# Performance work log

Measured on AMD Instinct MI355X. Metric: run time of the kernel, lower is better.

The kernel has to match this reference:

```python
import jax, jax.numpy as jnp
import numpy as np

DIM = 512
HEADS = 8
HEAD_DIM = 64
MAX_FREQ = 256.0


def axial_freqs(H, W, head_dim, max_freq=MAX_FREQ):
    # rotary-embedding-torch: per-axis rotary dim = head_dim // 2, freqs_for='pixel'
    r = head_dim // 2
    base = jnp.linspace(1.0, max_freq / 2.0, r // 2) * jnp.pi  # (r/2,)
    ph = jnp.linspace(-1.0, 1.0, H)
    pw = jnp.linspace(-1.0, 1.0, W)
    fh = jnp.repeat(ph[:, None] * base[None, :], 2, axis=-1)  # (H, r) interleaved repeat
    fw = jnp.repeat(pw[:, None] * base[None, :], 2, axis=-1)  # (W, r)
    fh = jnp.broadcast_to(fh[:, None, :], (H, W, r))
    fw = jnp.broadcast_to(fw[None, :, :], (H, W, r))
    return jnp.concatenate([fh, fw], axis=-1)  # (H, W, head_dim)


def rotate_half(t):
    # interleaved pairs: (x1, x2) -> (-x2, x1)
    shp = t.shape
    t = t.reshape(*shp[:-1], -1, 2)
    return jnp.stack((-t[..., 1], t[..., 0]), axis=-1).reshape(shp)


def apply_rope(t, freqs):
    # freqs: (H, W, d) broadcast over (BT, h, H, W, d)
    return t * jnp.cos(freqs) + rotate_half(t) * jnp.sin(freqs)


def setup_inputs() -> dict:
    key = jax.random.key(0)
    k1, k2, k3 = jax.random.split(key, 3)
    B, T, H, W, D = 2, 8, 32, 32, DIM
    inner = HEADS * HEAD_DIM
    x = jax.random.normal(k1, (B, T, H, W, D), dtype=jnp.float32)
    w_qkv = jax.random.normal(k2, (3 * inner, D), dtype=jnp.float32) * (D ** -0.5)
    w_out = jax.random.normal(k3, (D, inner), dtype=jnp.float32) * (inner ** -0.5)
    b_out = jnp.zeros((D,), dtype=jnp.float32)
    return {"x": x, "w_qkv": w_qkv, "w_out": w_out, "b_out": b_out}


def reference(x, w_qkv, w_out, b_out):
    B, T, H, W, D = x.shape
    h, d = HEADS, HEAD_DIM
    qkv = jnp.einsum('bthwc,fc->bthwf', x, w_qkv)  # (B,T,H,W,3*inner)
    q, k, v = jnp.split(qkv, 3, axis=-1)

    def to_heads(t):
        # B T H W (h d) -> (B T) h H W d
        t = t.reshape(B * T, H, W, h, d)
        return jnp.transpose(t, (0, 3, 1, 2, 4))

    q, k, v = to_heads(q), to_heads(k), to_heads(v)
    freqs = axial_freqs(H, W, d)
    q = apply_rope(q, freqs)
    k = apply_rope(k, freqs)

    q = q.reshape(B * T, h, H * W, d)
    k = k.reshape(B * T, h, H * W, d)
    v = v.reshape(B * T, h, H * W, d)

    scale = d ** -0.5
    logits = jnp.einsum('bhnd,bhmd->bhnm', q, k) * scale
    attn = jax.nn.softmax(logits, axis=-1)
    out = jnp.einsum('bhnm,bhmd->bhnd', attn, v)  # (BT, h, HW, d)

    # (B T) h (H W) d -> B T H W (h d)
    out = out.reshape(B, T, h, H, W, d)
    out = jnp.transpose(out, (0, 1, 3, 4, 2, 5)).reshape(B, T, H, W, h * d)
    return jnp.einsum('bthwf,df->bthwd', out, w_out) + b_out
```

## Files before the change

kernel.cpp:

```cpp
#include <hip/hip_runtime.h>
#include <math.h>

#define NH 8
#define HD 64
#define NSEQ 1024
#define DMODEL 512
#define F3 1536
#define NTOK 16384
#define BH 128
#define KVP 72
#define TP 136
#define QSCALE 0.1803368867f

typedef __attribute__((ext_vector_type(8))) short bf16x8;
typedef __attribute__((ext_vector_type(4))) float f32x4;
typedef __attribute__((ext_vector_type(16))) float f32x16;
typedef __attribute__((ext_vector_type(4))) unsigned int u32x4;
#define MFMA16(a, b, c) __builtin_amdgcn_mfma_f32_16x16x32_bf16(a, b, c, 0, 0, 0)
#define MFMA32(a, b, c) __builtin_amdgcn_mfma_f32_32x32x16_bf16(a, b, c, 0, 0, 0)

__device__ __forceinline__ float freq_of(int j) {
    return 3.14159265358979323846f * (1.0f + (float)j * (127.0f / 15.0f));
}
__device__ __forceinline__ unsigned short bf16_hi(float x) {
    unsigned u = __builtin_bit_cast(unsigned, x);
    return (unsigned short)(u >> 16);
}
__device__ __forceinline__ unsigned short bf16_rtn(float x) {
    unsigned u = __builtin_bit_cast(unsigned, x);
    return (unsigned short)((u + 0x7FFF + ((u >> 16) & 1)) >> 16);
}
__device__ __forceinline__ float bf16_tofloat(unsigned short h) {
    unsigned u = ((unsigned)h) << 16;
    return __builtin_bit_cast(float, u);
}
__device__ __forceinline__ int swz(int r) { return (r & 3) ^ ((r >> 2) & 3); }

__global__ __launch_bounds__(256) void split_kernel(
        const float* __restrict__ src, unsigned short* __restrict__ hi,
        unsigned short* __restrict__ lo) {
    const int i = blockIdx.x * 256 + threadIdx.x;
    const float4 v = ((const float4*)src)[i];
    ushort4 h, l;
    h.x = bf16_hi(v.x); l.x = bf16_hi(v.x - bf16_tofloat(h.x));
    h.y = bf16_hi(v.y); l.y = bf16_hi(v.y - bf16_tofloat(h.y));
    h.z = bf16_hi(v.z); l.z = bf16_hi(v.z - bf16_tofloat(h.z));
    h.w = bf16_hi(v.w); l.w = bf16_hi(v.w - bf16_tofloat(h.w));
    ((ushort4*)hi)[i] = h;
    ((ushort4*)lo)[i] = l;
}
__global__ __launch_bounds__(256) void cvt_kernel(
        const float* __restrict__ src, unsigned short* __restrict__ dst) {
    const int i = blockIdx.x * 256 + threadIdx.x;
    const float4 v = ((const float4*)src)[i];
    ((ushort4*)dst)[i] = make_ushort4(bf16_rtn(v.x), bf16_rtn(v.y),
                                      bf16_rtn(v.z), bf16_rtn(v.w));
}

template<int PLANES>
__device__ __forceinline__ void gemm_reg_pipe(
        const unsigned short* __restrict__ a_hi, const unsigned short* __restrict__ a_lo,
        const unsigned short* __restrict__ b_bf,
        char* lds, int m0, int f0, int t, f32x4 acc[4][4]) {
    const int w = t >> 6, lane = t & 63, l15 = lane & 15, quad = lane >> 4;
    const int mw = (w & 1) * 64, nw = (w >> 1) * 64;
    const int STAGE = PLANES * 4096;
    const int r = t >> 1;
    const int g0 = (t & 1) * 2;

    uint4 regs[PLANES][2];
    auto load_regs = [&](int kt) {
        const int k0 = kt * 32;
        #pragma unroll
        for (int p = 0; p < PLANES; p++) {
            const unsigned short* src =
                (p == 0) ? a_hi : ((p == PLANES - 1) ? b_bf : a_lo);
            const int row0 = (p == PLANES - 1) ? f0 : m0;
            const unsigned short* g = src + (size_t)(row0 + r) * DMODEL + k0 + g0 * 8;
            regs[p][0] = *(const uint4*)g;
            regs[p][1] = *(const uint4*)(g + 8);
        }
    };
    auto store_lds = [&](int stage) {
        unsigned short* S = (unsigned short*)lds + stage * STAGE;
        const int s0 = ((g0 ^ swz(r))) * 8;
        const int s1 = (((g0 + 1) ^ swz(r))) * 8;
        #pragma unroll
        for (int p = 0; p < PLANES; p++) {
            unsigned short* Sp = S + p * 4096 + r * 32;
            *(uint4*)&Sp[s0] = regs[p][0];
            *(uint4*)&Sp[s1] = regs[p][1];
        }
    };

    load_regs(0);
    store_lds(0);
    for (int kt = 0; kt < 16; kt++) {
        __syncthreads();
        if (kt < 15) load_regs(kt + 1);
        const unsigned short* S = (const unsigned short*)lds + (kt & 1) * STAGE;
        bf16x8 ah[4], al[4], bb[4];
        #pragma unroll
        for (int mt = 0; mt < 4; mt++) {
            const int rr = mw + mt * 16 + l15;
            const int off = rr * 32 + (quad ^ swz(rr)) * 8;
            ah[mt] = *(const bf16x8*)&S[off];
            if (PLANES == 3) al[mt] = *(const bf16x8*)&S[4096 + off];
        }
        #pragma unroll
        for (int nt = 0; nt < 4; nt++) {
            const int rr = nw + nt * 16 + l15;
            bb[nt] = *(const bf16x8*)&S[(PLANES - 1) * 4096 + rr * 32
                                        + (quad ^ swz(rr)) * 8];
        }
        #pragma unroll
        for (int mt = 0; mt < 4; mt++)
            #pragma unroll
            for (int nt = 0; nt < 4; nt++) {
                acc[mt][nt] = MFMA16(ah[mt], bb[nt], acc[mt][nt]);
                if (PLANES == 3) acc[mt][nt] = MFMA16(al[mt], bb[nt], acc[mt][nt]);
            }
        if (kt < 15) store_lds((kt + 1) & 1);
    }
    __syncthreads();
}

__global__ __launch_bounds__(256, 3) void qkv_mfma_kernel(
        const unsigned short* __restrict__ x_hi, const unsigned short* __restrict__ x_lo,
        const unsigned short* __restrict__ wq_bf,
        unsigned short* __restrict__ q_bf, unsigned short* __restrict__ k_bf,
        unsigned short* __restrict__ v_th) {
    __shared__ __align__(16) char lds[49152 + 4608];
    unsigned short* T = (unsigned short*)lds;
    float* t_cy = (float*)(lds + 49152);
    float* t_sy = t_cy + 64;
    float* t_cx = t_sy + 64;
    float* t_sx = t_cx + 512;

    const int m0 = blockIdx.x * 128;
    const int f0 = blockIdx.y * 128;
    const int t = threadIdx.x;
    const int w = t >> 6, lane = t & 63, l15 = lane & 15, quad = lane >> 4;
    const int mw = (w & 1) * 64, nw = (w >> 1) * 64;
    const int sel = f0 >> 9;
    const int bt = m0 >> 10;
    const int n0 = m0 & 1023;

    if (sel != 2) {
        for (int idx = t; idx < 576; idx += 256) {
            if (idx < 64) {
                const int yi = idx >> 4, j = idx & 15;
                const float pos = -1.0f + (float)((n0 >> 5) + yi) * (2.0f / 31.0f);
                float sv, cv; sincosf(pos * freq_of(j), &sv, &cv);
                t_sy[idx] = sv; t_cy[idx] = cv;
            } else {
                const int k2 = idx - 64, xi = k2 >> 4, j = k2 & 15;
                const float pos = -1.0f + (float)xi * (2.0f / 31.0f);
                float sv, cv; sincosf(pos * freq_of(j), &sv, &cv);
                t_sx[k2] = sv; t_cx[k2] = cv;
            }
        }
    }
    __syncthreads();

    f32x4 acc[4][4];
    #pragma unroll
    for (int mt = 0; mt < 4; mt++)
        #pragma unroll
        for (int nt = 0; nt < 4; nt++) acc[mt][nt] = (f32x4){0.f, 0.f, 0.f, 0.f};

    gemm_reg_pipe<3>(x_hi, x_lo, wq_bf, lds, m0, f0, t, acc);

    if (sel != 2) {
        const float post = (sel == 0) ? QSCALE : 1.0f;
        #pragma unroll
        for (int mt = 0; mt < 4; mt++)
            #pragma unroll
            for (int nt = 0; nt < 4; nt++)
                #pragma unroll
                for (int rr = 0; rr < 4; rr++) {
                    const int ml = mw + mt * 16 + quad * 4 + rr;
                    const int dd = (nw + nt * 16 + l15) & 63;
                    const int j0 = (dd & 31) >> 1;
                    float c, s;
                    if (dd < 32) { c = t_cy[(ml >> 5) * 16 + j0]; s = t_sy[(ml >> 5) * 16 + j0]; }
                    else         { c = t_cx[(ml & 31) * 16 + j0]; s = t_sx[(ml & 31) * 16 + j0]; }
                    const float v = acc[mt][nt][rr];
                    const float pv = __shfl_xor(v, 1);
                    acc[mt][nt][rr] = ((l15 & 1) ? (v * c + pv * s) : (v * c - pv * s)) * post;
                }
    }

    if (sel == 2) {
        #pragma unroll
        for (int mt = 0; mt < 4; mt++)
            #pragma unroll
            for (int nt = 0; nt < 4; nt++) {
                const int fl = nw + nt * 16 + l15;
                const int mlb = mw + mt * 16 + quad * 4;
                ushort4 pk = make_ushort4(
                    bf16_rtn(acc[mt][nt][0]), bf16_rtn(acc[mt][nt][1]),
                    bf16_rtn(acc[mt][nt][2]), bf16_rtn(acc[mt][nt][3]));
                *(ushort4*)&T[fl * TP + mlb] = pk;
            }
    } else {
        #pragma unroll
        for (int mt = 0; mt < 4; mt++)
            #pragma unroll
            for (int nt = 0; nt < 4; nt++)
                #pragma unroll
                for (int rr = 0; rr < 4; rr++) {
                    const int ml = mw + mt * 16 + quad * 4 + rr;
                    const int fl = nw + nt * 16 + l15;
                    T[ml * TP + fl] = bf16_rtn(acc[mt][nt][rr]);
                }
    }
    __syncthreads();
    if (sel == 2) {
        #pragma unroll
        for (int p = 0; p < 8; p++) {
            const int idx = p * 256 + t;
            const int fl = idx >> 4, g8 = (idx & 15) * 8;
            const int head = ((f0 + fl) >> 6) & 7;
            *(uint4*)(v_th + ((size_t)(bt * NH + head) * HD + ((f0 + fl) & 63)) * NSEQ
                      + n0 + g8) = *(const uint4*)&T[fl * TP + g8];
        }
    } else {
        unsigned short* dst = (sel == 0) ? q_bf : k_bf;
        #pragma unroll
        for (int p = 0; p < 8; p++) {
            const int idx = p * 256 + t;
            const int ml = idx >> 4, g8 = (idx & 15) * 8;
            const int head = ((f0 + g8) >> 6) & 7;
            *(uint4*)(dst + ((size_t)(bt * NH + head) * NSEQ + n0 + ml) * HD
                      + ((f0 + g8) & 63)) = *(const uint4*)&T[ml * TP + g8];
        }
    }
    __syncthreads();
}

__global__ __launch_bounds__(256, 3) void attn_kernel(
        const unsigned short* __restrict__ q_bf, const unsigned short* __restrict__ k_bf,
        const unsigned short* __restrict__ v_th,
        unsigned short* __restrict__ o_bf) {
    __shared__ unsigned short Ks[2][64 * KVP];
    __shared__ unsigned short Vs[2][64 * KVP];

    const int bh = blockIdx.x;
    const int qt = blockIdx.y;
    const int t = threadIdx.x;
    const int w = t >> 6;
    const int lane = t & 63;
    const int l31 = lane & 31;
    const int hi = lane >> 5;

    const size_t bh_nd = (size_t)bh * NSEQ * HD;
    const size_t bh_dn = (size_t)bh * HD * NSEQ;

    bf16x8 qfB[4];
    {
        const size_t rbase = bh_nd + (size_t)(qt * 128 + w * 32 + l31) * HD + hi * 8;
        #pragma unroll
        for (int ds = 0; ds < 4; ds++)
            qfB[ds] = *(const bf16x8*)(q_bf + rbase + ds * 16);
    }

    uint4 kr[2], vr[2];
    auto load_kv = [&](int kt) {
        #pragma unroll
        for (int p = 0; p < 2; p++) {
            const int cc = t + p * 256;
            const int r = cc >> 3, off8 = (cc & 7) * 8;
            kr[p] = *(const uint4*)(k_bf + bh_nd + (size_t)(kt * 64 + r) * HD + off8);
            vr[p] = *(const uint4*)(v_th + bh_dn + (size_t)r * NSEQ + kt * 64 + off8);
        }
    };
    auto store_kv = [&](int st) {
        #pragma unroll
        for (int p = 0; p < 2; p++) {
            const int cc = t + p * 256;
            const int r = cc >> 3, off8 = (cc & 7) * 8;
            *(uint4*)&Ks[st][r * KVP + off8] = kr[p];
            *(uint4*)&Vs[st][r * KVP + off8] = vr[p];
        }
    };

    const bf16x8 ones = {(short)0x3F80, (short)0x3F80, (short)0x3F80, (short)0x3F80,
                         (short)0x3F80, (short)0x3F80, (short)0x3F80, (short)0x3F80};

    f32x16 o_acc[2], l_acc;
    #pragma unroll
    for (int i = 0; i < 16; i++) {
        o_acc[0][i] = 0.f; o_acc[1][i] = 0.f; l_acc[i] = 0.f;
    }

    load_kv(0);
    store_kv(0);
    for (int kt = 0; kt < 16; kt++) {
        __syncthreads();
        if (kt < 15) load_kv(kt + 1);
        const unsigned short* K = Ks[kt & 1];
        const unsigned short* V = Vs[kt & 1];

        #pragma unroll
        for (int nt2 = 0; nt2 < 2; nt2++) {
            f32x16 s;
            #pragma unroll
            for (int i = 0; i < 16; i++) s[i] = 0.f;
            #pragma unroll
            for (int ds = 0; ds < 4; ds++) {
                const bf16x8 kb =
                    *(const bf16x8*)&K[(nt2 * 32 + l31) * KVP + ds * 16 + hi * 8];
                s = MFMA32(kb, qfB[ds], s);
            }

            unsigned wv[8];
            #pragma unroll
            for (int i = 0; i < 8; i++) {
                const float p0 = exp2f(s[2 * i]);
                const float p1 = exp2f(s[2 * i + 1]);
                asm("v_cvt_pk_bf16_f32 %0, %1, %2" : "=v"(wv[i]) : "v"(p0), "v"(p1));
            }
            asm volatile("v_permlane32_swap_b32 %0, %1" : "+v"(wv[0]), "+v"(wv[2]));
            asm volatile("v_permlane32_swap_b32 %0, %1" : "+v"(wv[1]), "+v"(wv[3]));
            asm volatile("v_permlane32_swap_b32 %0, %1" : "+v"(wv[4]), "+v"(wv[6]));
            asm volatile("v_permlane32_swap_b32 %0, %1" : "+v"(wv[5]), "+v"(wv[7]));

            #pragma unroll
            for (int k2 = 0; k2 < 2; k2++) {
                const u32x4 paw = {wv[k2 * 4 + 0], wv[k2 * 4 + 1],
                                   wv[k2 * 4 + 2], wv[k2 * 4 + 3]};
                const bf16x8 pa = __builtin_bit_cast(bf16x8, paw);
                const int kstep = nt2 * 2 + k2;
                l_acc = MFMA32(pa, ones, l_acc);
                #pragma unroll
                for (int dt = 0; dt < 2; dt++) {
                    const bf16x8 vb =
                        *(const bf16x8*)&V[(dt * 32 + l31) * KVP + kstep * 16 + hi * 8];
                    o_acc[dt] = MFMA32(pa, vb, o_acc[dt]);
                }
            }
        }
        if (kt < 15) store_kv((kt + 1) & 1);
    }

    const int btq = bh >> 3, head = bh & 7;
    #pragma unroll
    for (int r = 0; r < 16; r++) {
        const float inv = 1.0f / l_acc[r];
        const int row = qt * 128 + w * 32 + (r & 3) + 8 * (r >> 2) + 4 * hi;
        #pragma unroll
        for (int dt = 0; dt < 2; dt++) {
            o_bf[((size_t)(btq * NSEQ + row)) * DMODEL + head * HD + dt * 32 + l31] =
                bf16_rtn(o_acc[dt][r] * inv);
        }
    }
}

__global__ __launch_bounds__(256, 3) void proj_mfma_kernel(
        const unsigned short* __restrict__ o_bf,
        const unsigned short* __restrict__ wo_bf,
        const float* __restrict__ b_out, float* __restrict__ out) {
    __shared__ __align__(16) char lds[32768];

    const int m0 = blockIdx.x * 128;
    const int f0 = blockIdx.y * 128;
    const int t = threadIdx.x;
    const int w = t >> 6, lane = t & 63, l15 = lane & 15, quad = lane >> 4;
    const int mw = (w & 1) * 64, nw = (w >> 1) * 64;

    f32x4 acc[4][4];
    #pragma unroll
    for (int mt = 0; mt < 4; mt++)
        #pragma unroll
        for (int nt = 0; nt < 4; nt++) acc[mt][nt] = (f32x4){0.f, 0.f, 0.f, 0.f};

    gemm_reg_pipe<2>(o_bf, o_bf, wo_bf, lds, m0, f0, t, acc);

    float bias_v[4];
    #pragma unroll
    for (int nt = 0; nt < 4; nt++) bias_v[nt] = b_out[f0 + nw + nt * 16 + l15];
    #pragma unroll
    for (int mt = 0; mt < 4; mt++)
        #pragma unroll
        for (int nt = 0; nt < 4; nt++)
            #pragma unroll
            for (int rr = 0; rr < 4; rr++) {
                const int m = m0 + mw + mt * 16 + quad * 4 + rr;
                out[(size_t)m * DMODEL + f0 + nw + nt * 16 + l15] =
                    acc[mt][nt][rr] + bias_v[nt];
            }
}

extern "C" void kernel_launch(void* const* d_in, const int* in_sizes, int n_in,
                              void* d_out, int out_size, void* d_ws, size_t ws_size,
                              hipStream_t stream) {
    const float* x  = (const float*)d_in[0];
    const float* wq = (const float*)d_in[1];
    const float* wo = (const float*)d_in[2];
    const float* bo = (const float*)d_in[3];
    float* out = (float*)d_out;

    const size_t per = (size_t)BH * NSEQ * HD;
    unsigned short* x_hi = (unsigned short*)d_ws;
    unsigned short* x_lo = x_hi + per;
    unsigned short* q_bf = x_lo + per;
    unsigned short* k_bf = q_bf + per;
    unsigned short* v_th = k_bf + per;
    unsigned short* wq_bf = v_th + per;
    unsigned short* wo_bf = wq_bf + (size_t)F3 * DMODEL;
    unsigned short* o_bf = x_hi;

    split_kernel<<<dim3((int)(per / 1024)), 256, 0, stream>>>(x, x_hi, x_lo);
    cvt_kernel<<<dim3(F3 * DMODEL / 1024), 256, 0, stream>>>(wq, wq_bf);
    cvt_kernel<<<dim3(DMODEL * DMODEL / 1024), 256, 0, stream>>>(wo, wo_bf);
    qkv_mfma_kernel<<<dim3(NTOK / 128, F3 / 128), 256, 0, stream>>>(
        x_hi, x_lo, wq_bf, q_bf, k_bf, v_th);
    attn_kernel<<<dim3(BH, 8), 256, 0, stream>>>(
        q_bf, k_bf, v_th, o_bf);
    proj_mfma_kernel<<<dim3(NTOK / 128, DMODEL / 128), 256, 0, stream>>>(
        o_bf, wo_bf, bo, out);
}
```

Measured before the change: 257.3 us.

## Widen QKV GEMM tile to 256 columns and stage attention output through LDS

```diff
diff --git a/kernel.cpp b/kernel.cpp
--- a/kernel.cpp
+++ b/kernel.cpp
@@ -57,25 +57,26 @@
                                       bf16_rtn(v.z), bf16_rtn(v.w));
 }
 
-template<int PLANES>
+template<int PLANES, int NREP>
 __device__ __forceinline__ void gemm_reg_pipe(
         const unsigned short* __restrict__ a_hi, const unsigned short* __restrict__ a_lo,
         const unsigned short* __restrict__ b_bf,
-        char* lds, int m0, int f0, int t, f32x4 acc[4][4]) {
+        char* lds, int m0, int f0, int t, f32x4 (&acc)[NREP][4][4]) {
     const int w = t >> 6, lane = t & 63, l15 = lane & 15, quad = lane >> 4;
     const int mw = (w & 1) * 64, nw = (w >> 1) * 64;
-    const int STAGE = PLANES * 4096;
+    const int APL = PLANES - 1;
+    const int NPL = APL + NREP;
+    const int STAGE = NPL * 4096;
     const int r = t >> 1;
     const int g0 = (t & 1) * 2;
 
-    uint4 regs[PLANES][2];
+    uint4 regs[NPL][2];
     auto load_regs = [&](int kt) {
         const int k0 = kt * 32;
         #pragma unroll
-        for (int p = 0; p < PLANES; p++) {
-            const unsigned short* src =
-                (p == 0) ? a_hi : ((p == PLANES - 1) ? b_bf : a_lo);
-            const int row0 = (p == PLANES - 1) ? f0 : m0;
+        for (int p = 0; p < NPL; p++) {
+            const unsigned short* src = (p < APL) ? (p == 0 ? a_hi : a_lo) : b_bf;
+            const int row0 = (p < APL) ? m0 : (f0 + (p - APL) * 128);
             const unsigned short* g = src + (size_t)(row0 + r) * DMODEL + k0 + g0 * 8;
             regs[p][0] = *(const uint4*)g;
             regs[p][1] = *(const uint4*)(g + 8);
@@ -86,7 +87,7 @@
         const int s0 = ((g0 ^ swz(r))) * 8;
         const int s1 = (((g0 + 1) ^ swz(r))) * 8;
         #pragma unroll
-        for (int p = 0; p < PLANES; p++) {
+        for (int p = 0; p < NPL; p++) {
             unsigned short* Sp = S + p * 4096 + r * 32;
             *(uint4*)&Sp[s0] = regs[p][0];
             *(uint4*)&Sp[s1] = regs[p][1];
@@ -99,46 +100,50 @@
         __syncthreads();
         if (kt < 15) load_regs(kt + 1);
         const unsigned short* S = (const unsigned short*)lds + (kt & 1) * STAGE;
-        bf16x8 ah[4], al[4], bb[4];
+        bf16x8 ah[4], al[4];
         #pragma unroll
         for (int mt = 0; mt < 4; mt++) {
             const int rr = mw + mt * 16 + l15;
             const int off = rr * 32 + (quad ^ swz(rr)) * 8;
             ah[mt] = *(const bf16x8*)&S[off];
-            if (PLANES == 3) al[mt] = *(const bf16x8*)&S[4096 + off];
-        }
-        #pragma unroll
-        for (int nt = 0; nt < 4; nt++) {
-            const int rr = nw + nt * 16 + l15;
-            bb[nt] = *(const bf16x8*)&S[(PLANES - 1) * 4096 + rr * 32
-                                        + (quad ^ swz(rr)) * 8];
-        }
-        #pragma unroll
-        for (int mt = 0; mt < 4; mt++)
+            if (APL == 2) al[mt] = *(const bf16x8*)&S[4096 + off];
+        }
+        #pragma unroll
+        for (int nr = 0; nr < NREP; nr++) {
+            bf16x8 bb[4];
             #pragma unroll
             for (int nt = 0; nt < 4; nt++) {
-                acc[mt][nt] = MFMA16(ah[mt], bb[nt], acc[mt][nt]);
-                if (PLANES == 3) acc[mt][nt] = MFMA16(al[mt], bb[nt], acc[mt][nt]);
-            }
+                const int rr = nw + nt * 16 + l15;
+                bb[nt] = *(const bf16x8*)&S[(APL + nr) * 4096 + rr * 32
+                                            + (quad ^ swz(rr)) * 8];
+            }
+            #pragma unroll
+            for (int mt = 0; mt < 4; mt++)
+                #pragma unroll
+                for (int nt = 0; nt < 4; nt++) {
+                    acc[nr][mt][nt] = MFMA16(ah[mt], bb[nt], acc[nr][mt][nt]);
+                    if (APL == 2) acc[nr][mt][nt] = MFMA16(al[mt], bb[nt], acc[nr][mt][nt]);
+                }
+        }
         if (kt < 15) store_lds((kt + 1) & 1);
     }
     __syncthreads();
 }
 
-__global__ __launch_bounds__(256, 3) void qkv_mfma_kernel(
+__global__ __launch_bounds__(256, 2) void qkv_mfma_kernel(
         const unsigned short* __restrict__ x_hi, const unsigned short* __restrict__ x_lo,
         const unsigned short* __restrict__ wq_bf,
         unsigned short* __restrict__ q_bf, unsigned short* __restrict__ k_bf,
         unsigned short* __restrict__ v_th) {
-    __shared__ __align__(16) char lds[49152 + 4608];
+    __shared__ __align__(16) char lds[65536 + 4608];
     unsigned short* T = (unsigned short*)lds;
-    float* t_cy = (float*)(lds + 49152);
+    float* t_cy = (float*)(lds + 65536);
     float* t_sy = t_cy + 64;
     float* t_cx = t_sy + 64;
     float* t_sx = t_cx + 512;
 
     const int m0 = blockIdx.x * 128;
-    const int f0 = blockIdx.y * 128;
+    const int f0 = blockIdx.y * 256;
     const int t = threadIdx.x;
     const int w = t >> 6, lane = t & 63, l15 = lane & 15, quad = lane >> 4;
     const int mw = (w & 1) * 64, nw = (w >> 1) * 64;
@@ -163,80 +168,87 @@
     }
     __syncthreads();
 
-    f32x4 acc[4][4];
-    #pragma unroll
-    for (int mt = 0; mt < 4; mt++)
-        #pragma unroll
-        for (int nt = 0; nt < 4; nt++) acc[mt][nt] = (f32x4){0.f, 0.f, 0.f, 0.f};
-
-    gemm_reg_pipe<3>(x_hi, x_lo, wq_bf, lds, m0, f0, t, acc);
-
-    if (sel != 2) {
-        const float post = (sel == 0) ? QSCALE : 1.0f;
+    f32x4 acc[2][4][4];
+    #pragma unroll
+    for (int nr = 0; nr < 2; nr++)
         #pragma unroll
         for (int mt = 0; mt < 4; mt++)
             #pragma unroll
-            for (int nt = 0; nt < 4; nt++)
+            for (int nt = 0; nt < 4; nt++) acc[nr][mt][nt] = (f32x4){0.f, 0.f, 0.f, 0.f};
+
+    gemm_reg_pipe<3, 2>(x_hi, x_lo, wq_bf, lds, m0, f0, t, acc);
+
+    #pragma unroll
+    for (int nr = 0; nr < 2; nr++) {
+        const int fs = f0 + nr * 128;
+        if (sel != 2) {
+            const float post = (sel == 0) ? QSCALE : 1.0f;
+            #pragma unroll
+            for (int mt = 0; mt < 4; mt++)
                 #pragma unroll
-                for (int rr = 0; rr < 4; rr++) {
-                    const int ml = mw + mt * 16 + quad * 4 + rr;
-                    const int dd = (nw + nt * 16 + l15) & 63;
-                    const int j0 = (dd & 31) >> 1;
-                    float c, s;
-                    if (dd < 32) { c = t_cy[(ml >> 5) * 16 + j0]; s = t_sy[(ml >> 5) * 16 + j0]; }
-                    else         { c = t_cx[(ml & 31) * 16 + j0]; s = t_sx[(ml & 31) * 16 + j0]; }
-                    const float v = acc[mt][nt][rr];
-                    const float pv = __shfl_xor(v, 1);
-                    acc[mt][nt][rr] = ((l15 & 1) ? (v * c + pv * s) : (v * c - pv * s)) * post;
+                for (int nt = 0; nt < 4; nt++)
+                    #pragma unroll
+                    for (int rr = 0; rr < 4; rr++) {
+                        const int ml = mw + mt * 16 + quad * 4 + rr;
+                        const int dd = (nw + nt * 16 + l15) & 63;
+                        const int j0 = (dd & 31) >> 1;
+                        float c, s;
+                        if (dd < 32) { c = t_cy[(ml >> 5) * 16 + j0]; s = t_sy[(ml >> 5) * 16 + j0]; }
+                        else         { c = t_cx[(ml & 31) * 16 + j0]; s = t_sx[(ml & 31) * 16 + j0]; }
+                        const float v = acc[nr][mt][nt][rr];
+                        const float pv = __shfl_xor(v, 1);
+                        acc[nr][mt][nt][rr] =
+                            ((l15 & 1) ? (v * c + pv * s) : (v * c - pv * s)) * post;
+                    }
+        }
+
+        if (sel == 2) {
+            #pragma unroll
+            for (int mt = 0; mt < 4; mt++)
+                #pragma unroll
+                for (int nt = 0; nt < 4; nt++) {
+                    const int fl = nw + nt * 16 + l15;
+                    const int mlb = mw + mt * 16 + quad * 4;
+                    ushort4 pk = make_ushort4(
+                        bf16_rtn(acc[nr][mt][nt][0]), bf16_rtn(acc[nr][mt][nt][1]),
+                        bf16_rtn(acc[nr][mt][nt][2]), bf16_rtn(acc[nr][mt][nt][3]));
+                    *(ushort4*)&T[fl * TP + mlb] = pk;
                 }
-    }
-
-    if (sel == 2) {
-        #pragma unroll
-        for (int mt = 0; mt < 4; mt++)
-            #pragma unroll
-            for (int nt = 0; nt < 4; nt++) {
-                const int fl = nw + nt * 16 + l15;
-                const int mlb = mw + mt * 16 + quad * 4;
-                ushort4 pk = make_ushort4(
-                    bf16_rtn(acc[mt][nt][0]), bf16_rtn(acc[mt][nt][1]),
-                    bf16_rtn(acc[mt][nt][2]), bf16_rtn(acc[mt][nt][3]));
-                *(ushort4*)&T[fl * TP + mlb] = pk;
-            }
-    } else {
-        #pragma unroll
-        for (int mt = 0; mt < 4; mt++)
-            #pragma unroll
-            for (int nt = 0; nt < 4; nt++)
+        } else {
+            #pragma unroll
+            for (int mt = 0; mt < 4; mt++)
                 #pragma unroll
-                for (int rr = 0; rr < 4; rr++) {
-                    const int ml = mw + mt * 16 + quad * 4 + rr;
-                    const int fl = nw + nt * 16 + l15;
-                    T[ml * TP + fl] = bf16_rtn(acc[mt][nt][rr]);
-                }
-    }
-    __syncthreads();
-    if (sel == 2) {
-        #pragma unroll
-        for (int p = 0; p < 8; p++) {
-            const int idx = p * 256 + t;
-            const int fl = idx >> 4, g8 = (idx & 15) * 8;
-            const int head = ((f0 + fl) >> 6) & 7;
-            *(uint4*)(v_th + ((size_t)(bt * NH + head) * HD + ((f0 + fl) & 63)) * NSEQ
-                      + n0 + g8) = *(const uint4*)&T[fl * TP + g8];
-        }
-    } else {
-        unsigned short* dst = (sel == 0) ? q_bf : k_bf;
-        #pragma unroll
-        for (int p = 0; p < 8; p++) {
-            const int idx = p * 256 + t;
-            const int ml = idx >> 4, g8 = (idx & 15) * 8;
-            const int head = ((f0 + g8) >> 6) & 7;
-            *(uint4*)(dst + ((size_t)(bt * NH + head) * NSEQ + n0 + ml) * HD
-                      + ((f0 + g8) & 63)) = *(const uint4*)&T[ml * TP + g8];
-        }
-    }
-    __syncthreads();
+                for (int nt = 0; nt < 4; nt++)
+                    #pragma unroll
+                    for (int rr = 0; rr < 4; rr++) {
+                        const int ml = mw + mt * 16 + quad * 4 + rr;
+                        const int fl = nw + nt * 16 + l15;
+                        T[ml * TP + fl] = bf16_rtn(acc[nr][mt][nt][rr]);
+                    }
+        }
+        __syncthreads();
+        if (sel == 2) {
+            #pragma unroll
+            for (int p = 0; p < 8; p++) {
+                const int idx = p * 256 + t;
+                const int fl = idx >> 4, g8 = (idx & 15) * 8;
+                const int head = ((fs + fl) >> 6) & 7;
+                *(uint4*)(v_th + ((size_t)(bt * NH + head) * HD + ((fs + fl) & 63)) * NSEQ
+                          + n0 + g8) = *(const uint4*)&T[fl * TP + g8];
+            }
+        } else {
+            unsigned short* dst = (sel == 0) ? q_bf : k_bf;
+            #pragma unroll
+            for (int p = 0; p < 8; p++) {
+                const int idx = p * 256 + t;
+                const int ml = idx >> 4, g8 = (idx & 15) * 8;
+                const int head = ((fs + g8) >> 6) & 7;
+                *(uint4*)(dst + ((size_t)(bt * NH + head) * NSEQ + n0 + ml) * HD
+                          + ((fs + g8) & 63)) = *(const uint4*)&T[ml * TP + g8];
+            }
+        }
+        __syncthreads();
+    }
 }
 
 __global__ __launch_bounds__(256, 3) void attn_kernel(
@@ -344,16 +356,24 @@
         if (kt < 15) store_kv((kt + 1) & 1);
     }
 
-    const int btq = bh >> 3, head = bh & 7;
+    __syncthreads();
+    unsigned short* Osh = &Ks[0][0];
     #pragma unroll
     for (int r = 0; r < 16; r++) {
         const float inv = 1.0f / l_acc[r];
-        const int row = qt * 128 + w * 32 + (r & 3) + 8 * (r >> 2) + 4 * hi;
-        #pragma unroll
-        for (int dt = 0; dt < 2; dt++) {
-            o_bf[((size_t)(btq * NSEQ + row)) * DMODEL + head * HD + dt * 32 + l31] =
-                bf16_rtn(o_acc[dt][r] * inv);
-        }
+        const int row = w * 32 + (r & 3) + 8 * (r >> 2) + 4 * hi;
+        #pragma unroll
+        for (int dt = 0; dt < 2; dt++)
+            Osh[row * KVP + dt * 32 + l31] = bf16_rtn(o_acc[dt][r] * inv);
+    }
+    __syncthreads();
+    const int btq = bh >> 3, head = bh & 7;
+    #pragma unroll
+    for (int p = 0; p < 4; p++) {
+        const int idx = p * 256 + t;
+        const int row = idx >> 3, g8 = (idx & 7) * 8;
+        *(uint4*)(o_bf + ((size_t)(btq * NSEQ + qt * 128 + row)) * DMODEL
+                  + head * HD + g8) = *(const uint4*)&Osh[row * KVP + g8];
     }
 }
 
@@ -369,13 +389,13 @@
     const int w = t >> 6, lane = t & 63, l15 = lane & 15, quad = lane >> 4;
     const int mw = (w & 1) * 64, nw = (w >> 1) * 64;
 
-    f32x4 acc[4][4];
+    f32x4 acc[1][4][4];
     #pragma unroll
     for (int mt = 0; mt < 4; mt++)
         #pragma unroll
-        for (int nt = 0; nt < 4; nt++) acc[mt][nt] = (f32x4){0.f, 0.f, 0.f, 0.f};
-
-    gemm_reg_pipe<2>(o_bf, o_bf, wo_bf, lds, m0, f0, t, acc);
+        for (int nt = 0; nt < 4; nt++) acc[0][mt][nt] = (f32x4){0.f, 0.f, 0.f, 0.f};
+
+    gemm_reg_pipe<2, 1>(o_bf, o_bf, wo_bf, lds, m0, f0, t, acc);
 
     float bias_v[4];
     #pragma unroll
@@ -388,7 +408,7 @@
             for (int rr = 0; rr < 4; rr++) {
                 const int m = m0 + mw + mt * 16 + quad * 4 + rr;
                 out[(size_t)m * DMODEL + f0 + nw + nt * 16 + l15] =
-                    acc[mt][nt][rr] + bias_v[nt];
+                    acc[0][mt][nt][rr] + bias_v[nt];
             }
 }
 
@@ -414,7 +434,7 @@
     split_kernel<<<dim3((int)(per / 1024)), 256, 0, stream>>>(x, x_hi, x_lo);
     cvt_kernel<<<dim3(F3 * DMODEL / 1024), 256, 0, stream>>>(wq, wq_bf);
     cvt_kernel<<<dim3(DMODEL * DMODEL / 1024), 256, 0, stream>>>(wo, wo_bf);
-    qkv_mfma_kernel<<<dim3(NTOK / 128, F3 / 128), 256, 0, stream>>>(
+    qkv_mfma_kernel<<<dim3(NTOK / 128, F3 / 256), 256, 0, stream>>>(
         x_hi, x_lo, wq_bf, q_bf, k_bf, v_th);
     attn_kernel<<<dim3(BH, 8), 256, 0, stream>>>(
         q_bf, k_bf, v_th, o_bf);
```

Measured after the change: 252.9 us. About the same (-1.7%).
